# Performance work log

Hardware: AMD Instinct MI355X
Metric: run time of the kernel (lower is better)

Reference implementation:

```python
import jax, jax.numpy as jnp
import numpy as np

N = 4096   # nodes per side
B = 32     # graphs per batch
E = 65536  # edges per side
D = 128    # hidden dim
L = 4      # layers
H = 4      # heads


def setup_inputs() -> dict:
    key = jax.random.key(0)
    ks = jax.random.split(key, 20)
    s = 1.0 / np.sqrt(D)
    inp = {
        'x_s': jax.random.normal(ks[0], (N, D), jnp.float32),
        'x_t': jax.random.normal(ks[1], (N, D), jnp.float32),
        'edge_index_s': jax.random.randint(ks[2], (2, E), 0, N),
        'edge_attr_s': jax.random.uniform(ks[3], (E, D), jnp.float32),
        'edge_index_t': jax.random.randint(ks[4], (2, E), 0, N),
        'edge_attr_t': jax.random.uniform(ks[5], (E, D), jnp.float32),
        'batch_s': jnp.repeat(jnp.arange(B), N // B),
        'batch_t': jnp.repeat(jnp.arange(B), N // B),
        # stacked per-layer parameters (torch Linear layout: [out, in])
        'gnn_rel_w': jax.random.normal(ks[6], (L, D, D), jnp.float32) * s,
        'gnn_rel_b': jnp.zeros((L, D), jnp.float32),
        'gnn_root_w': jax.random.normal(ks[7], (L, D, D), jnp.float32) * s,
        'attn_in_w': jax.random.normal(ks[8], (L, 3 * D, D), jnp.float32) * s,
        'attn_in_b': jnp.zeros((L, 3 * D), jnp.float32),
        'attn_out_w': jax.random.normal(ks[9], (L, D, D), jnp.float32) * s,
        'attn_out_b': jnp.zeros((L, D), jnp.float32),
        'ln_g': jnp.ones((L, D), jnp.float32),
        'ln_b': jnp.zeros((L, D), jnp.float32),
        'gate_w': jax.random.normal(ks[10], (D, 1), jnp.float32) * s,
        'gate_b': jnp.zeros((1,), jnp.float32),
    }
    return inp


def _graph_conv(x, src, dst, ew, w_rel, b_rel, w_root):
    # message = edge_weight * x_j, aggr='mean' over target nodes
    msg = ew * x[src]                                   # [E, D]
    agg = jax.ops.segment_sum(msg, dst, num_segments=N)
    cnt = jax.ops.segment_sum(jnp.ones((msg.shape[0], 1), x.dtype), dst, num_segments=N)
    mean = agg / jnp.maximum(cnt, 1.0)
    return mean @ w_rel.T + b_rel + x @ w_root.T


def _mha(qx, kx, w_in, b_in, w_out, b_out, mask):
    dh = D // H
    q = (qx @ w_in[:D].T + b_in[:D]).reshape(-1, H, dh)
    k = (kx @ w_in[D:2 * D].T + b_in[D:2 * D]).reshape(-1, H, dh)
    v = (kx @ w_in[2 * D:].T + b_in[2 * D:]).reshape(-1, H, dh)
    scores = jnp.einsum('qhd,khd->hqk', q, k) * (1.0 / np.sqrt(dh))
    scores = jnp.where(mask[None], -jnp.inf, scores)
    a = jax.nn.softmax(scores, axis=-1)
    o = jnp.einsum('hqk,khd->qhd', a, v).reshape(-1, D)
    return o @ w_out.T + b_out


def _layernorm(x, g, b, eps=1e-5):
    mu = jnp.mean(x, axis=-1, keepdims=True)
    var = jnp.mean((x - mu) ** 2, axis=-1, keepdims=True)
    return (x - mu) * jax.lax.rsqrt(var + eps) * g + b


def _pool(x, batch, gw, gb):
    # GlobalAttention: gate = sigmoid(Linear(x)); softmax per graph; weighted sum
    gate = jax.nn.sigmoid(x @ gw + gb)                  # [N, 1]
    m = jax.ops.segment_max(gate, batch, num_segments=B)
    e = jnp.exp(gate - m[batch])
    z = jax.ops.segment_sum(e, batch, num_segments=B)
    alpha = e / z[batch]
    return jax.ops.segment_sum(alpha * x, batch, num_segments=B)  # [B, D]


def reference(x_s, x_t, edge_index_s, edge_attr_s, edge_index_t, edge_attr_t,
              batch_s, batch_t, gnn_rel_w, gnn_rel_b, gnn_root_w,
              attn_in_w, attn_in_b, attn_out_w, attn_out_b, ln_g, ln_b,
              gate_w, gate_b):
    src_s, dst_s = edge_index_s[0], edge_index_s[1]
    src_t, dst_t = edge_index_t[0], edge_index_t[1]
    mask = batch_s[:, None] != batch_t[None, :]         # True = blocked
    for i in range(L):
        x_s = _graph_conv(x_s, src_s, dst_s, edge_attr_s, gnn_rel_w[i], gnn_rel_b[i], gnn_root_w[i])
        x_t = _graph_conv(x_t, src_t, dst_t, edge_attr_t, gnn_rel_w[i], gnn_rel_b[i], gnn_root_w[i])
        o_s = _mha(x_s, x_t, attn_in_w[i], attn_in_b[i], attn_out_w[i], attn_out_b[i], mask)
        o_t = _mha(x_t, x_s, attn_in_w[i], attn_in_b[i], attn_out_w[i], attn_out_b[i], mask.T)
        x_s = _layernorm(o_s, ln_g[i], ln_b[i])
        x_t = _layernorm(o_t, ln_g[i], ln_b[i])
    p_s = _pool(x_s, batch_s, gate_w, gate_b)
    p_t = _pool(x_t, batch_t, gate_w, gate_b)
    p_s = p_s / jnp.maximum(jnp.linalg.norm(p_s, axis=-1, keepdims=True), 1e-12)
    p_t = p_t / jnp.maximum(jnp.linalg.norm(p_t, axis=-1, keepdims=True), 1e-12)
    return jnp.sum(p_s * p_t, axis=-1)                  # [B]
```

## Files before the change

### kernel.cpp

```cpp
#include <hip/hip_runtime.h>
#include <math.h>

#define N_NODES 4096
#define NROWS   8192
#define BGRAPH  32
#define NEDGE   65536
#define DIM     128
#define NLAYER  4
#define NHEAD   4
#define DHEAD   32
#define QDIM    384

typedef _Float16 half8v __attribute__((ext_vector_type(8)));
typedef _Float16 half4v __attribute__((ext_vector_type(4)));
typedef _Float16 half2v __attribute__((ext_vector_type(2)));
typedef float f32x4 __attribute__((ext_vector_type(4)));

__device__ inline f32x4 MFMA(half8v a, half8v b, f32x4 c) {
    return __builtin_amdgcn_mfma_f32_16x16x32_f16(a, b, c, 0, 0, 0);
}

__device__ inline void cvt4(const float* __restrict__ s, _Float16* __restrict__ d, int i) {
    float4 v = ((const float4*)s)[i];
    half4v h;
    h[0] = (_Float16)v.x; h[1] = (_Float16)v.y;
    h[2] = (_Float16)v.z; h[3] = (_Float16)v.w;
    *(half4v*)(d + (size_t)i * 4) = h;
}

__global__ __launch_bounds__(256) void cvth_kernel(
    const float* __restrict__ x_s, const float* __restrict__ x_t,
    const float* __restrict__ out_w,
    const int* __restrict__ dst_s, const int* __restrict__ dst_t,
    _Float16* __restrict__ x16, _Float16* __restrict__ outw16,
    int* __restrict__ cnt)
{
    int gid = blockIdx.x * 256 + threadIdx.x, gs = gridDim.x * 256;
    const int nx = N_NODES * DIM / 4;
    const int nw = NLAYER * DIM * DIM / 4;
    for (int i = gid; i < nx; i += gs) cvt4(x_s, x16, i);
    for (int i = gid; i < nx; i += gs) cvt4(x_t, x16 + N_NODES * DIM, i);
    for (int i = gid; i < nw; i += gs) cvt4(out_w, outw16, i);
    for (int i = gid; i < 2 * NEDGE; i += gs) {
        int side = i >> 16, e = i & (NEDGE - 1);
        const int* dd = side ? dst_t : dst_s;
        atomicAdd(&cnt[side * N_NODES + dd[e]], 1);
    }
}

__global__ __launch_bounds__(256) void scan_kernel(
    const int* __restrict__ cnt, int* __restrict__ row_start, int* __restrict__ cursor)
{
    int side = blockIdx.x;
    int t = threadIdx.x;
    __shared__ int part[256];
    int local[16];
    int s = 0;
    #pragma unroll
    for (int j = 0; j < 16; ++j) { local[j] = cnt[side * N_NODES + t * 16 + j]; s += local[j]; }
    part[t] = s;
    __syncthreads();
    for (int off = 1; off < 256; off <<= 1) {
        int v = (t >= off) ? part[t - off] : 0;
        __syncthreads();
        part[t] += v;
        __syncthreads();
    }
    int run = (t == 0) ? 0 : part[t - 1];
    #pragma unroll
    for (int j = 0; j < 16; ++j) {
        int idx = t * 16 + j;
        row_start[side * (N_NODES + 1) + idx] = run;
        cursor[side * N_NODES + idx] = run;
        run += local[j];
    }
    if (t == 255) row_start[side * (N_NODES + 1) + N_NODES] = run;
}

__global__ __launch_bounds__(256) void rg_kernel(
    const int* __restrict__ src_s, const int* __restrict__ dst_s,
    const int* __restrict__ src_t, const int* __restrict__ dst_t,
    const float* __restrict__ ea_s, const float* __restrict__ ea_t,
    int* __restrict__ cursor, int* __restrict__ srcs, _Float16* __restrict__ ea16s)
{
    int t = threadIdx.x;
    int g16 = t >> 4, sub = t & 15, lane = t & 63;
    int ef = blockIdx.x * 16 + g16;
    int side = ef >> 16, e = ef & (NEDGE - 1);
    const int* dd = side ? dst_t : dst_s;
    const int* ss = side ? src_t : src_s;
    const float* ea = side ? ea_t : ea_s;
    int pos = 0;
    if (sub == 0) pos = atomicAdd(&cursor[side * N_NODES + dd[e]], 1);
    pos = __shfl(pos, lane & ~15);
    if (sub == 0) srcs[side * NEDGE + pos] = ss[e];
    const float* sp = ea + (size_t)e * DIM + sub * 8;
    float4 v0 = *(const float4*)(sp);
    float4 v1 = *(const float4*)(sp + 4);
    half8v h;
    h[0]=(_Float16)v0.x; h[1]=(_Float16)v0.y; h[2]=(_Float16)v0.z; h[3]=(_Float16)v0.w;
    h[4]=(_Float16)v1.x; h[5]=(_Float16)v1.y; h[6]=(_Float16)v1.z; h[7]=(_Float16)v1.w;
    *(half8v*)(ea16s + (size_t)(side * NEDGE + pos) * DIM + sub * 8) = h;
}

__global__ __launch_bounds__(256) void wprod_kernel(
    const float* __restrict__ in_w, const float* __restrict__ root_w,
    const float* __restrict__ rel_w, const float* __restrict__ rel_b,
    const float* __restrict__ in_b,
    _Float16* __restrict__ wq16, float* __restrict__ beff)
{
    int gid = blockIdx.x * 256 + threadIdx.x;
    const int MT = NLAYER * 2 * QDIM * DIM;
    if (gid < MT) {
        int L = gid / (2 * QDIM * DIM);
        int r = gid % (2 * QDIM * DIM);
        int m = r / (QDIM * DIM);
        int r2 = r % (QDIM * DIM);
        int i = r2 / DIM, k = r2 % DIM;
        const float* Win = in_w + (size_t)L * QDIM * DIM;
        const float* B = (m ? rel_w : root_w) + (size_t)L * DIM * DIM;
        float s = 0.f;
        #pragma unroll 4
        for (int j = 0; j < DIM; ++j) s += Win[i * DIM + j] * B[j * DIM + k];
        wq16[gid] = (_Float16)s;
    } else {
        int r = gid - MT;
        if (r >= NLAYER * QDIM) return;
        int L = r / QDIM, i = r % QDIM;
        const float* Win = in_w + (size_t)L * QDIM * DIM;
        const float* br = rel_b + (size_t)L * DIM;
        float s = in_b[(size_t)L * QDIM + i];
        #pragma unroll 4
        for (int j = 0; j < DIM; ++j) s += Win[i * DIM + j] * br[j];
        beff[r] = s;
    }
}

__global__ __launch_bounds__(64) void agg_kernel(
    const int* __restrict__ srcs, const _Float16* __restrict__ ea16s,
    const int* __restrict__ row_start,
    const _Float16* __restrict__ x16, _Float16* __restrict__ agg16)
{
    int n = blockIdx.x, side = blockIdx.y;
    int lane = threadIdx.x;
    const int* sp = srcs + side * NEDGE;
    const _Float16* ep = ea16s + (size_t)side * NEDGE * DIM + lane * 2;
    const _Float16* xp = x16 + (size_t)side * N_NODES * DIM + lane * 2;
    int rs = row_start[side * (N_NODES + 1) + n];
    int re = row_start[side * (N_NODES + 1) + n + 1];
    float ax = 0.f, ay = 0.f;
    int i = rs;
    for (; i + 2 <= re; i += 2) {
        int s0 = sp[i], s1 = sp[i + 1];
        half2v w0 = *(const half2v*)(ep + (size_t)i * DIM);
        half2v w1 = *(const half2v*)(ep + (size_t)(i + 1) * DIM);
        half2v x0 = *(const half2v*)(xp + (size_t)s0 * DIM);
        half2v x1 = *(const half2v*)(xp + (size_t)s1 * DIM);
        ax += (float)w0[0] * (float)x0[0] + (float)w1[0] * (float)x1[0];
        ay += (float)w0[1] * (float)x0[1] + (float)w1[1] * (float)x1[1];
    }
    if (i < re) {
        int s0 = sp[i];
        half2v w0 = *(const half2v*)(ep + (size_t)i * DIM);
        half2v x0 = *(const half2v*)(xp + (size_t)s0 * DIM);
        ax += (float)w0[0] * (float)x0[0];
        ay += (float)w0[1] * (float)x0[1];
    }
    float sc = 1.0f / (float)max(re - rs, 1);
    half2v o; o[0] = (_Float16)(ax * sc); o[1] = (_Float16)(ay * sc);
    *(half2v*)(agg16 + (size_t)(side * N_NODES + n) * DIM + lane * 2) = o;
}

__global__ __launch_bounds__(256) void qkv2_mfma(
    const _Float16* __restrict__ x16, const _Float16* __restrict__ agg16,
    const _Float16* __restrict__ wq,
    const float* __restrict__ beff,
    _Float16* __restrict__ qb16)
{
    int tid = threadIdx.x;
    int wave = tid >> 6, lane = tid & 63;
    int wm = wave >> 1, wn = wave & 1;
    int row0 = blockIdx.x * 64 + wm * 32;
    int col0 = blockIdx.y * 64 + wn * 32;
    int lr = lane & 15;
    int lk = (lane >> 4) * 8;
    f32x4 zero = {0.f, 0.f, 0.f, 0.f};
    f32x4 acc[2][2] = {{zero, zero}, {zero, zero}};
    #pragma unroll
    for (int s = 0; s < 2; ++s) {
        const _Float16* A = s ? agg16 : x16;
        const _Float16* W = wq + (size_t)s * QDIM * DIM;
        const _Float16* Ap0 = A + (size_t)(row0 + lr) * DIM + lk;
        const _Float16* Ap1 = A + (size_t)(row0 + 16 + lr) * DIM + lk;
        const _Float16* Wp0 = W + (size_t)(col0 + lr) * DIM + lk;
        const _Float16* Wp1 = W + (size_t)(col0 + 16 + lr) * DIM + lk;
        #pragma unroll
        for (int k0 = 0; k0 < DIM; k0 += 32) {
            half8v a0 = *(const half8v*)(Ap0 + k0);
            half8v a1 = *(const half8v*)(Ap1 + k0);
            half8v b0 = *(const half8v*)(Wp0 + k0);
            half8v b1 = *(const half8v*)(Wp1 + k0);
            acc[0][0] = MFMA(a0, b0, acc[0][0]);
            acc[0][1] = MFMA(a0, b1, acc[0][1]);
            acc[1][0] = MFMA(a1, b0, acc[1][0]);
            acc[1][1] = MFMA(a1, b1, acc[1][1]);
        }
    }
    int g4 = (lane >> 4) * 4;
    #pragma unroll
    for (int fc = 0; fc < 2; ++fc) {
        int col = col0 + fc * 16 + lr;
        float bv = beff[col];
        #pragma unroll
        for (int fr = 0; fr < 2; ++fr) {
            int rbase = row0 + fr * 16 + g4;
            #pragma unroll
            for (int j = 0; j < 4; ++j) {
                float v = acc[fr][fc][j] + bv;
                qb16[(size_t)(rbase + j) * QDIM + col] = (_Float16)v;
            }
        }
    }
}

__global__ __launch_bounds__(256) void attn_oln_kernel(
    const _Float16* __restrict__ qkv, const _Float16* __restrict__ outw,
    const float* __restrict__ bias, const float* __restrict__ gamma,
    const float* __restrict__ beta, _Float16* __restrict__ x16out)
{
    int g = blockIdx.x, dir = blockIdx.y, rb = blockIdx.z;
    int qoff  = dir ? N_NODES : 0;
    int kvoff = dir ? 0 : N_NODES;
    int t = threadIdx.x;
    int w = t >> 6, lane = t & 63;
    int lr = lane & 15, g4 = lane >> 4;
    __shared__ _Float16 VT[NHEAD][32][136];
    __shared__ _Float16 P[NHEAD][16][136];
    __shared__ float red_s[16][5], red_q[16][5];
    f32x4 zero = {0.f, 0.f, 0.f, 0.f};
    for (int kk = lane; kk < 128; kk += 64) {
        const _Float16* vp = qkv + (size_t)(kvoff + g * 128 + kk) * QDIM + 2 * DIM + w * DHEAD;
        half8v v0 = *(const half8v*)(vp);
        half8v v1 = *(const half8v*)(vp + 8);
        half8v v2 = *(const half8v*)(vp + 16);
        half8v v3 = *(const half8v*)(vp + 24);
        #pragma unroll
        for (int j = 0; j < 8; ++j) {
            VT[w][j][kk]      = v0[j];
            VT[w][8 + j][kk]  = v1[j];
            VT[w][16 + j][kk] = v2[j];
            VT[w][24 + j][kk] = v3[j];
        }
    }
    int qrow0 = qoff + g * 128 + rb * 16;
    const _Float16* qp = qkv + (size_t)(qrow0 + lr) * QDIM + w * DHEAD + g4 * 8;
    half8v qfrag = *(const half8v*)qp;
    f32x4 S[8];
    #pragma unroll
    for (int kf = 0; kf < 8; ++kf) {
        const _Float16* kp = qkv + (size_t)(kvoff + g * 128 + kf * 16 + lr) * QDIM
                             + DIM + w * DHEAD + g4 * 8;
        S[kf] = MFMA(qfrag, *(const half8v*)kp, zero);
    }
    const float scale = 0.17677669529663687f;
    #pragma unroll
    for (int j = 0; j < 4; ++j) {
        float m = -INFINITY;
        #pragma unroll
        for (int kf = 0; kf < 8; ++kf) m = fmaxf(m, S[kf][j]);
        m *= scale;
        #pragma unroll
        for (int mk = 1; mk < 16; mk <<= 1) m = fmaxf(m, __shfl_xor(m, mk));
        float pj[8];
        float l = 0.f;
        #pragma unroll
        for (int kf = 0; kf < 8; ++kf) {
            float pv = __expf(S[kf][j] * scale - m);
            pj[kf] = pv; l += pv;
        }
        #pragma unroll
        for (int mk = 1; mk < 16; mk <<= 1) l += __shfl_xor(l, mk);
        float linv = 1.0f / l;
        int row = g4 * 4 + j;
        #pragma unroll
        for (int kf = 0; kf < 8; ++kf)
            P[w][row][kf * 16 + lr] = (_Float16)(pj[kf] * linv);
    }
    f32x4 O[2] = {zero, zero};
    #pragma unroll
    for (int ks = 0; ks < 4; ++ks) {
        half8v pa = *(const half8v*)&P[w][lr][ks * 32 + g4 * 8];
        #pragma unroll
        for (int df = 0; df < 2; ++df) {
            half8v vb = *(const half8v*)&VT[w][df * 16 + lr][ks * 32 + g4 * 8];
            O[df] = MFMA(pa, vb, O[df]);
        }
    }
    __syncthreads();
    _Float16 (*OL)[136] = P[0];
    #pragma unroll
    for (int df = 0; df < 2; ++df)
        #pragma unroll
        for (int j = 0; j < 4; ++j)
            OL[g4 * 4 + j][w * DHEAD + df * 16 + lr] = (_Float16)O[df][j];
    __syncthreads();
    f32x4 acc2[2] = {zero, zero};
    #pragma unroll
    for (int kk = 0; kk < 4; ++kk) {
        half8v a = *(const half8v*)&OL[lr][kk * 32 + g4 * 8];
        #pragma unroll
        for (int ct = 0; ct < 2; ++ct) {
            const _Float16* wp = outw + (size_t)(w * 32 + ct * 16 + lr) * DIM + kk * 32 + g4 * 8;
            acc2[ct] = MFMA(a, *(const half8v*)wp, acc2[ct]);
        }
    }
    float v[2][4];
    #pragma unroll
    for (int ct = 0; ct < 2; ++ct) {
        float bv = bias[w * 32 + ct * 16 + lr];
        #pragma unroll
        for (int j = 0; j < 4; ++j) v[ct][j] = acc2[ct][j] + bv;
    }
    #pragma unroll
    for (int j = 0; j < 4; ++j) {
        float ss = v[0][j] + v[1][j];
        float qq = v[0][j] * v[0][j] + v[1][j] * v[1][j];
        #pragma unroll
        for (int mk = 1; mk < 16; mk <<= 1) {
            ss += __shfl_xor(ss, mk);
            qq += __shfl_xor(qq, mk);
        }
        if (lr == 0) {
            red_s[g4 * 4 + j][w] = ss;
            red_q[g4 * 4 + j][w] = qq;
        }
    }
    __syncthreads();
    #pragma unroll
    for (int j = 0; j < 4; ++j) {
        int row = g4 * 4 + j;
        float Sv = red_s[row][0] + red_s[row][1] + red_s[row][2] + red_s[row][3];
        float Qv = red_q[row][0] + red_q[row][1] + red_q[row][2] + red_q[row][3];
        float mu = Sv * (1.0f / 128.0f);
        float inv = rsqrtf(Qv * (1.0f / 128.0f) - mu * mu + 1e-5f);
        #pragma unroll
        for (int ct = 0; ct < 2; ++ct) {
            int col = w * 32 + ct * 16 + lr;
            float o = (v[ct][j] - mu) * inv * gamma[col] + beta[col];
            x16out[(size_t)(qrow0 + row) * DIM + col] = (_Float16)o;
        }
    }
}

__global__ __launch_bounds__(256) void poolcos_kernel(
    const _Float16* __restrict__ x16, const float* __restrict__ gw,
    const float* __restrict__ gb, float* __restrict__ out)
{
    int g = blockIdx.x, t = threadIdx.x;
    int side = t >> 7, r = t & 127;
    __shared__ float sm[2][128];
    __shared__ float al[2][128];
    __shared__ float pl[2][DIM];
    const _Float16* xr = x16 + (size_t)(side * N_NODES + g * 128 + r) * DIM;
    float dot = gb[0];
    #pragma unroll
    for (int d = 0; d < DIM; d += 8) {
        half8v xv = *(const half8v*)(xr + d);
        #pragma unroll
        for (int u = 0; u < 8; ++u) dot += (float)xv[u] * gw[d + u];
    }
    float gate = 1.0f / (1.0f + __expf(-dot));
    sm[side][r] = gate; __syncthreads();
    for (int sN = 64; sN > 0; sN >>= 1) {
        if (r < sN) sm[side][r] = fmaxf(sm[side][r], sm[side][r + sN]);
        __syncthreads();
    }
    float m = sm[side][0]; __syncthreads();
    float e = __expf(gate - m);
    sm[side][r] = e; __syncthreads();
    for (int sN = 64; sN > 0; sN >>= 1) {
        if (r < sN) sm[side][r] += sm[side][r + sN];
        __syncthreads();
    }
    al[side][r] = e / sm[side][0];
    __syncthreads();
    int d = t & 127;
    float acc = 0.0f;
    const _Float16* xg = x16 + (size_t)(side * N_NODES + g * 128) * DIM;
    for (int n = 0; n < 128; ++n) acc += al[side][n] * (float)xg[(size_t)n * DIM + d];
    pl[side][d] = acc;
    __syncthreads();
    if (t < 64) {
        float a0 = pl[0][t], a1 = pl[0][64 + t];
        float b0 = pl[1][t], b1 = pl[1][64 + t];
        float saa = a0 * a0 + a1 * a1;
        float sbb = b0 * b0 + b1 * b1;
        float sab = a0 * b0 + a1 * b1;
        #pragma unroll
        for (int off = 32; off; off >>= 1) {
            saa += __shfl_down(saa, off);
            sbb += __shfl_down(sbb, off);
            sab += __shfl_down(sab, off);
        }
        if (t == 0) {
            float na = fmaxf(sqrtf(saa), 1e-12f);
            float nb = fmaxf(sqrtf(sbb), 1e-12f);
            out[g] = sab / (na * nb);
        }
    }
}

extern "C" void kernel_launch(void* const* d_in, const int* in_sizes, int n_in,
                              void* d_out, int out_size, void* d_ws, size_t ws_size,
                              hipStream_t stream)
{
    const float* x_s    = (const float*)d_in[0];
    const float* x_t    = (const float*)d_in[1];
    const int*   ei_s   = (const int*)d_in[2];
    const float* ea_s   = (const float*)d_in[3];
    const int*   ei_t   = (const int*)d_in[4];
    const float* ea_t   = (const float*)d_in[5];
    const float* rel_w  = (const float*)d_in[8];
    const float* rel_b  = (const float*)d_in[9];
    const float* root_w = (const float*)d_in[10];
    const float* in_w   = (const float*)d_in[11];
    const float* in_b   = (const float*)d_in[12];
    const float* out_w  = (const float*)d_in[13];
    const float* out_b  = (const float*)d_in[14];
    const float* g_ln   = (const float*)d_in[15];
    const float* b_ln   = (const float*)d_in[16];
    const float* gate_w = (const float*)d_in[17];
    const float* gate_b = (const float*)d_in[18];
    float* out = (float*)d_out;

    const size_t RD = (size_t)NROWS * DIM;
    _Float16* h16p = (_Float16*)d_ws;
    _Float16* x16    = h16p; h16p += RD;
    _Float16* agg16  = h16p; h16p += RD;
    _Float16* qb16   = h16p; h16p += RD * 3;
    _Float16* ea16s  = h16p; h16p += (size_t)2 * NEDGE * DIM;
    _Float16* outw16 = h16p; h16p += (size_t)NLAYER * DIM * DIM;
    _Float16* wq16   = h16p; h16p += (size_t)NLAYER * 2 * QDIM * DIM;
    float* fws = (float*)h16p;
    float* beff = fws; fws += NLAYER * QDIM;
    int* iws = (int*)fws;
    int* cnt       = iws; iws += 2 * N_NODES;
    int* cursor    = iws; iws += 2 * N_NODES;
    int* row_start = iws; iws += 2 * (N_NODES + 1);
    int* srcs      = iws; iws += 2 * NEDGE;

    const int* src_s = ei_s, *dst_s = ei_s + NEDGE;
    const int* src_t = ei_t, *dst_t = ei_t + NEDGE;

    hipMemsetAsync(cnt, 0, 2 * N_NODES * 4, stream);
    cvth_kernel<<<512, 256, 0, stream>>>(x_s, x_t, out_w, dst_s, dst_t,
                                         x16, outw16, cnt);
    scan_kernel<<<2, 256, 0, stream>>>(cnt, row_start, cursor);
    rg_kernel<<<2 * NEDGE / 16, 256, 0, stream>>>(src_s, dst_s, src_t, dst_t,
                                                  ea_s, ea_t, cursor, srcs, ea16s);
    wprod_kernel<<<(NLAYER * 2 * QDIM * DIM + NLAYER * QDIM + 255) / 256, 256, 0, stream>>>(
        in_w, root_w, rel_w, rel_b, in_b, wq16, beff);

    dim3 gq(NROWS / 64, QDIM / 64);
    dim3 gagg(N_NODES, 2);
    dim3 gattn(BGRAPH, 2, 8);

    for (int i = 0; i < NLAYER; ++i) {
        const _Float16* wq   = wq16   + (size_t)i * 2 * QDIM * DIM;
        const float*    be   = beff   + (size_t)i * QDIM;
        const _Float16* wout = outw16 + (size_t)i * DIM * DIM;
        const float*    bout = out_b  + (size_t)i * DIM;
        const float*    lg   = g_ln   + (size_t)i * DIM;
        const float*    lb   = b_ln   + (size_t)i * DIM;

        agg_kernel<<<gagg, 64, 0, stream>>>(srcs, ea16s, row_start, x16, agg16);
        qkv2_mfma<<<gq, 256, 0, stream>>>(x16, agg16, wq, be, qb16);
        attn_oln_kernel<<<gattn, 256, 0, stream>>>(qb16, wout, bout, lg, lb, x16);
    }

    poolcos_kernel<<<BGRAPH, 256, 0, stream>>>(x16, gate_w, gate_b, out);
}
```

Baseline: 213.0 us.

## Fold weight products with MFMA and widen edge aggregation to 16-byte lanes

```diff
diff --git a/kernel.cpp b/kernel.cpp
--- a/kernel.cpp
+++ b/kernel.cpp
@@ -28,19 +28,29 @@
     *(half4v*)(d + (size_t)i * 4) = h;
 }
 
-__global__ __launch_bounds__(256) void cvth_kernel(
+__global__ __launch_bounds__(256) void cvt16_kernel(
     const float* __restrict__ x_s, const float* __restrict__ x_t,
-    const float* __restrict__ out_w,
+    const float* __restrict__ out_w, const float* __restrict__ in_w,
+    const float* __restrict__ root_w, const float* __restrict__ rel_w,
     const int* __restrict__ dst_s, const int* __restrict__ dst_t,
     _Float16* __restrict__ x16, _Float16* __restrict__ outw16,
+    _Float16* __restrict__ in16, _Float16* __restrict__ bt16,
     int* __restrict__ cnt)
 {
     int gid = blockIdx.x * 256 + threadIdx.x, gs = gridDim.x * 256;
     const int nx = N_NODES * DIM / 4;
     const int nw = NLAYER * DIM * DIM / 4;
+    const int ni = NLAYER * QDIM * DIM / 4;
     for (int i = gid; i < nx; i += gs) cvt4(x_s, x16, i);
     for (int i = gid; i < nx; i += gs) cvt4(x_t, x16 + N_NODES * DIM, i);
     for (int i = gid; i < nw; i += gs) cvt4(out_w, outw16, i);
+    for (int i = gid; i < ni; i += gs) cvt4(in_w, in16, i);
+    const int nb = NLAYER * 2 * DIM * DIM;
+    for (int i = gid; i < nb; i += gs) {
+        int j = i & 127, k = (i >> 7) & 127, m = (i >> 14) & 1, L = i >> 15;
+        const float* B = (m ? rel_w : root_w) + (size_t)L * DIM * DIM;
+        bt16[i] = (_Float16)B[j * DIM + k];
+    }
     for (int i = gid; i < 2 * NEDGE; i += gs) {
         int side = i >> 16, e = i & (NEDGE - 1);
         const int* dd = side ? dst_t : dst_s;
@@ -103,72 +113,104 @@
     *(half8v*)(ea16s + (size_t)(side * NEDGE + pos) * DIM + sub * 8) = h;
 }
 
-__global__ __launch_bounds__(256) void wprod_kernel(
-    const float* __restrict__ in_w, const float* __restrict__ root_w,
-    const float* __restrict__ rel_w, const float* __restrict__ rel_b,
-    const float* __restrict__ in_b,
-    _Float16* __restrict__ wq16, float* __restrict__ beff)
+__global__ __launch_bounds__(256) void wfold_mfma(
+    const _Float16* __restrict__ in16, const _Float16* __restrict__ bt16,
+    _Float16* __restrict__ wq16)
+{
+    int lm = blockIdx.z;
+    const _Float16* A = in16 + (size_t)(lm >> 1) * QDIM * DIM;
+    const _Float16* B = bt16 + (size_t)lm * DIM * DIM;
+    _Float16* C = wq16 + (size_t)lm * QDIM * DIM;
+    int tid = threadIdx.x;
+    int wave = tid >> 6, lane = tid & 63;
+    int wm = wave >> 1, wn = wave & 1;
+    int row0 = blockIdx.x * 64 + wm * 32;
+    int col0 = blockIdx.y * 64 + wn * 32;
+    int lr = lane & 15;
+    int lk = (lane >> 4) * 8;
+    f32x4 zero = {0.f, 0.f, 0.f, 0.f};
+    f32x4 acc[2][2] = {{zero, zero}, {zero, zero}};
+    const _Float16* Ap0 = A + (size_t)(row0 + lr) * DIM + lk;
+    const _Float16* Ap1 = A + (size_t)(row0 + 16 + lr) * DIM + lk;
+    const _Float16* Bp0 = B + (size_t)(col0 + lr) * DIM + lk;
+    const _Float16* Bp1 = B + (size_t)(col0 + 16 + lr) * DIM + lk;
+    #pragma unroll
+    for (int k0 = 0; k0 < DIM; k0 += 32) {
+        half8v a0 = *(const half8v*)(Ap0 + k0);
+        half8v a1 = *(const half8v*)(Ap1 + k0);
+        half8v b0 = *(const half8v*)(Bp0 + k0);
+        half8v b1 = *(const half8v*)(Bp1 + k0);
+        acc[0][0] = MFMA(a0, b0, acc[0][0]);
+        acc[0][1] = MFMA(a0, b1, acc[0][1]);
+        acc[1][0] = MFMA(a1, b0, acc[1][0]);
+        acc[1][1] = MFMA(a1, b1, acc[1][1]);
+    }
+    int g4 = (lane >> 4) * 4;
+    #pragma unroll
+    for (int fc = 0; fc < 2; ++fc) {
+        int col = col0 + fc * 16 + lr;
+        #pragma unroll
+        for (int fr = 0; fr < 2; ++fr) {
+            int rbase = row0 + fr * 16 + g4;
+            #pragma unroll
+            for (int j = 0; j < 4; ++j)
+                C[(size_t)(rbase + j) * DIM + col] = (_Float16)acc[fr][fc][j];
+        }
+    }
+}
+
+__global__ __launch_bounds__(256) void beff_kernel(
+    const float* __restrict__ in_w, const float* __restrict__ in_b,
+    const float* __restrict__ rel_b, float* __restrict__ beff)
 {
     int gid = blockIdx.x * 256 + threadIdx.x;
-    const int MT = NLAYER * 2 * QDIM * DIM;
-    if (gid < MT) {
-        int L = gid / (2 * QDIM * DIM);
-        int r = gid % (2 * QDIM * DIM);
-        int m = r / (QDIM * DIM);
-        int r2 = r % (QDIM * DIM);
-        int i = r2 / DIM, k = r2 % DIM;
-        const float* Win = in_w + (size_t)L * QDIM * DIM;
-        const float* B = (m ? rel_w : root_w) + (size_t)L * DIM * DIM;
-        float s = 0.f;
-        #pragma unroll 4
-        for (int j = 0; j < DIM; ++j) s += Win[i * DIM + j] * B[j * DIM + k];
-        wq16[gid] = (_Float16)s;
-    } else {
-        int r = gid - MT;
-        if (r >= NLAYER * QDIM) return;
-        int L = r / QDIM, i = r % QDIM;
-        const float* Win = in_w + (size_t)L * QDIM * DIM;
-        const float* br = rel_b + (size_t)L * DIM;
-        float s = in_b[(size_t)L * QDIM + i];
-        #pragma unroll 4
-        for (int j = 0; j < DIM; ++j) s += Win[i * DIM + j] * br[j];
-        beff[r] = s;
-    }
-}
-
-__global__ __launch_bounds__(64) void agg_kernel(
+    if (gid >= NLAYER * QDIM) return;
+    int L = gid / QDIM, i = gid % QDIM;
+    const float* Win = in_w + (size_t)L * QDIM * DIM;
+    const float* br = rel_b + (size_t)L * DIM;
+    float s = in_b[(size_t)L * QDIM + i];
+    #pragma unroll 4
+    for (int j = 0; j < DIM; ++j) s += Win[(size_t)i * DIM + j] * br[j];
+    beff[gid] = s;
+}
+
+__global__ __launch_bounds__(256) void agg_kernel(
     const int* __restrict__ srcs, const _Float16* __restrict__ ea16s,
     const int* __restrict__ row_start,
     const _Float16* __restrict__ x16, _Float16* __restrict__ agg16)
 {
-    int n = blockIdx.x, side = blockIdx.y;
-    int lane = threadIdx.x;
-    const int* sp = srcs + side * NEDGE;
-    const _Float16* ep = ea16s + (size_t)side * NEDGE * DIM + lane * 2;
-    const _Float16* xp = x16 + (size_t)side * N_NODES * DIM + lane * 2;
-    int rs = row_start[side * (N_NODES + 1) + n];
-    int re = row_start[side * (N_NODES + 1) + n + 1];
-    float ax = 0.f, ay = 0.f;
-    int i = rs;
-    for (; i + 2 <= re; i += 2) {
-        int s0 = sp[i], s1 = sp[i + 1];
-        half2v w0 = *(const half2v*)(ep + (size_t)i * DIM);
-        half2v w1 = *(const half2v*)(ep + (size_t)(i + 1) * DIM);
-        half2v x0 = *(const half2v*)(xp + (size_t)s0 * DIM);
-        half2v x1 = *(const half2v*)(xp + (size_t)s1 * DIM);
-        ax += (float)w0[0] * (float)x0[0] + (float)w1[0] * (float)x1[0];
-        ay += (float)w0[1] * (float)x0[1] + (float)w1[1] * (float)x1[1];
-    }
-    if (i < re) {
-        int s0 = sp[i];
-        half2v w0 = *(const half2v*)(ep + (size_t)i * DIM);
-        half2v x0 = *(const half2v*)(xp + (size_t)s0 * DIM);
-        ax += (float)w0[0] * (float)x0[0];
-        ay += (float)w0[1] * (float)x0[1];
-    }
-    float sc = 1.0f / (float)max(re - rs, 1);
-    half2v o; o[0] = (_Float16)(ax * sc); o[1] = (_Float16)(ay * sc);
-    *(half2v*)(agg16 + (size_t)(side * N_NODES + n) * DIM + lane * 2) = o;
+    int t = threadIdx.x;
+    int wid = t >> 6, lane = t & 63;
+    int sub = lane & 15, qe = lane >> 4;
+    int wg = blockIdx.x * 4 + wid;
+    for (int node = wg; node < NROWS; node += 2048) {
+        int side = node >> 12, n = node & (N_NODES - 1);
+        const int* sp = srcs + side * NEDGE;
+        const _Float16* ep = ea16s + (size_t)side * NEDGE * DIM + sub * 8;
+        const _Float16* xp = x16 + (size_t)side * N_NODES * DIM + sub * 8;
+        int rs = row_start[side * (N_NODES + 1) + n];
+        int re = row_start[side * (N_NODES + 1) + n + 1];
+        float acc[8] = {};
+        for (int i = rs + qe; i < re; i += 4) {
+            int s = sp[i];
+            half8v w = *(const half8v*)(ep + (size_t)i * DIM);
+            half8v xv = *(const half8v*)(xp + (size_t)s * DIM);
+            #pragma unroll
+            for (int j = 0; j < 8; ++j) acc[j] += (float)w[j] * (float)xv[j];
+        }
+        #pragma unroll
+        for (int j = 0; j < 8; ++j) {
+            acc[j] += __shfl_xor(acc[j], 16);
+            acc[j] += __shfl_xor(acc[j], 32);
+        }
+        if (qe == 0) {
+            float sc = 1.0f / (float)max(re - rs, 1);
+            half8v o;
+            #pragma unroll
+            for (int j = 0; j < 8; ++j) o[j] = (_Float16)(acc[j] * sc);
+            *(half8v*)(agg16 + (size_t)node * DIM + sub * 8) = o;
+        }
+    }
 }
 
 __global__ __launch_bounds__(256) void qkv2_mfma(
@@ -441,6 +483,8 @@
     _Float16* ea16s  = h16p; h16p += (size_t)2 * NEDGE * DIM;
     _Float16* outw16 = h16p; h16p += (size_t)NLAYER * DIM * DIM;
     _Float16* wq16   = h16p; h16p += (size_t)NLAYER * 2 * QDIM * DIM;
+    _Float16* in16   = h16p; h16p += (size_t)NLAYER * QDIM * DIM;
+    _Float16* bt16   = h16p; h16p += (size_t)NLAYER * 2 * DIM * DIM;
     float* fws = (float*)h16p;
     float* beff = fws; fws += NLAYER * QDIM;
     int* iws = (int*)fws;
@@ -453,16 +497,18 @@
     const int* src_t = ei_t, *dst_t = ei_t + NEDGE;
 
     hipMemsetAsync(cnt, 0, 2 * N_NODES * 4, stream);
-    cvth_kernel<<<512, 256, 0, stream>>>(x_s, x_t, out_w, dst_s, dst_t,
-                                         x16, outw16, cnt);
+    cvt16_kernel<<<512, 256, 0, stream>>>(x_s, x_t, out_w, in_w, root_w, rel_w,
+                                          dst_s, dst_t, x16, outw16, in16, bt16, cnt);
     scan_kernel<<<2, 256, 0, stream>>>(cnt, row_start, cursor);
     rg_kernel<<<2 * NEDGE / 16, 256, 0, stream>>>(src_s, dst_s, src_t, dst_t,
                                                   ea_s, ea_t, cursor, srcs, ea16s);
-    wprod_kernel<<<(NLAYER * 2 * QDIM * DIM + NLAYER * QDIM + 255) / 256, 256, 0, stream>>>(
-        in_w, root_w, rel_w, rel_b, in_b, wq16, beff);
+    {
+        dim3 gw(QDIM / 64, DIM / 64, NLAYER * 2);
+        wfold_mfma<<<gw, 256, 0, stream>>>(in16, bt16, wq16);
+    }
+    beff_kernel<<<(NLAYER * QDIM + 255) / 256, 256, 0, stream>>>(in_w, in_b, rel_b, beff);
 
     dim3 gq(NROWS / 64, QDIM / 64);
-    dim3 gagg(N_NODES, 2);
     dim3 gattn(BGRAPH, 2, 8);
 
     for (int i = 0; i < NLAYER; ++i) {
@@ -473,7 +519,7 @@
         const float*    lg   = g_ln   + (size_t)i * DIM;
         const float*    lb   = b_ln   + (size_t)i * DIM;
 
-        agg_kernel<<<gagg, 64, 0, stream>>>(srcs, ea16s, row_start, x16, agg16);
+        agg_kernel<<<512, 256, 0, stream>>>(srcs, ea16s, row_start, x16, agg16);
         qkv2_mfma<<<gq, 256, 0, stream>>>(x16, agg16, wq, be, qb16);
         attn_oln_kernel<<<gattn, 256, 0, stream>>>(qb16, wout, bout, lg, lb, x16);
     }
```

New measurement: 226.8 us. +6.5%, slower.
